# Kernel tuning notes

Hardware: AMD Instinct MI355X
Metric: run time of the kernel (lower is better)

Reference implementation:

```python
import jax, jax.numpy as jnp
import numpy as np

B, T, V, E, H, DE = 64, 52, 10000, 512, 512, 2048


def _lstm_cell(x, h, c, w_ih, w_hh, b_ih, b_hh):
    # torch.nn.LSTMCell gate order: i, f, g, o
    gates = x @ w_ih.T + h @ w_hh.T + b_ih + b_hh
    i, f, g, o = jnp.split(gates, 4, axis=-1)
    c2 = jax.nn.sigmoid(f) * c + jax.nn.sigmoid(i) * jnp.tanh(g)
    h2 = jax.nn.sigmoid(o) * jnp.tanh(c2)
    return h2, c2


def _run_dir(emb_seq, img, lens, p1, p2, fc_w, fc_b):
    # emb_seq: [B, Td, E]; img: [B, H]; lens: [B] sorted descending.
    # The torch loop slices h[:batch_size_t]; since lens is sorted descending,
    # that is equivalent to masking updates where t >= (len-1). Rows that fall
    # out of the active prefix are never read again, and their predictions stay 0.
    Bd, Td = emb_seq.shape[0], emb_seq.shape[1]
    Hd = img.shape[1]
    mask = jnp.arange(Td)[None, :] < (lens - 1)[:, None]  # [B, Td]
    z = jnp.zeros((Bd, Hd), emb_seq.dtype)

    def step(carry, xs):
        h, c, h1, c1 = carry
        x, m = xs
        m2 = m[:, None]
        hn, cn = _lstm_cell(x, h, c, *p1)
        h1n, c1n = _lstm_cell(jnp.concatenate([hn, img], axis=1), h1, c1, *p2)
        carry = (jnp.where(m2, hn, h), jnp.where(m2, cn, c),
                 jnp.where(m2, h1n, h1), jnp.where(m2, c1n, c1))
        preds = jnp.where(m2, h1n @ fc_w.T + fc_b, 0.0)  # [B, V]
        return carry, preds

    _, preds = jax.lax.scan(step, (z, z, z, z), (emb_seq.transpose(1, 0, 2), mask.T))
    return preds.transpose(1, 0, 2)  # [B, Td, V]


def setup_inputs():
    key = jax.random.key(0)
    ks = iter(jax.random.split(key, 48))

    def u(shape, a=-0.1, b=0.1):
        return jax.random.uniform(next(ks), shape, minval=a, maxval=b, dtype=jnp.float32)

    inp = {}
    inp['encoder_out'] = jax.random.normal(next(ks), (B, DE), dtype=jnp.float32)
    inp['encoded_captions'] = jax.random.randint(next(ks), (B, T), 0, V)
    cl = jax.random.randint(next(ks), (B, 1), 2, T + 1)
    inp['caption_lengths'] = cl.at[0, 0].set(T)  # ensure max decode length = T-1
    # embeddings (uniform -0.1..0.1 per init_weights)
    inp['emb_w'] = u((V, E))
    inp['emb_r_w'] = u((V, E))
    # LSTM cells: torch default init uniform(-1/sqrt(H), 1/sqrt(H))
    kH = 1.0 / np.sqrt(H)
    for name, din in [('1', E), ('2', 2 * H), ('r1', E), ('r2', 2 * H)]:
        inp['w_ih' + name] = u((4 * H, din), -kH, kH)
        inp['w_hh' + name] = u((4 * H, H), -kH, kH)
        inp['b_ih' + name] = u((4 * H,), -kH, kH)
        inp['b_hh' + name] = u((4 * H,), -kH, kH)
    kD = 1.0 / np.sqrt(DE)
    inp['img_f_w'] = u((H, DE), -kD, kD)
    inp['img_f_b'] = u((H,), -kD, kD)
    inp['img_b_w'] = u((H, DE), -kD, kD)
    inp['img_b_b'] = u((H,), -kD, kD)
    inp['fc_w'] = u((V, H))
    inp['fc_b'] = jnp.zeros((V,), jnp.float32)
    inp['fcr_w'] = u((V, H))
    inp['fcr_b'] = jnp.zeros((V,), jnp.float32)
    return inp


def reference(encoder_out, encoded_captions, caption_lengths, emb_w, emb_r_w,
              w_ih1, w_hh1, b_ih1, b_hh1, w_ih2, w_hh2, b_ih2, b_hh2,
              w_ihr1, w_hhr1, b_ihr1, b_hhr1, w_ihr2, w_hhr2, b_ihr2, b_hhr2,
              img_f_w, img_f_b, img_b_w, img_b_b, fc_w, fc_b, fcr_w, fcr_b):
    lens = caption_lengths[:, 0]
    order = jnp.argsort(-lens)  # descending, stable (jax argsort is stable)
    lens = lens[order]
    enc = encoder_out[order]
    caps = encoded_captions[order]
    Tc = caps.shape[1]
    # per-row reversal of the first len tokens; rest zero (matches torch loop)
    j = jnp.arange(Tc)[None, :]
    valid = j < lens[:, None]
    rev_idx = jnp.where(valid, lens[:, None] - 1 - j, 0)
    caps_rev = jnp.where(valid, jnp.take_along_axis(caps, rev_idx, axis=1), 0)
    emb = emb_w[caps]          # [B, T, E]
    emb_r = emb_r_w[caps_rev]  # [B, T, E]
    img_f = enc @ img_f_w.T + img_f_b
    img_r = enc @ img_b_w.T + img_b_b
    Td = Tc - 1  # max(decode_lengths); setup guarantees max(lens) == T
    preds = _run_dir(emb[:, :Td], img_f, lens,
                     (w_ih1, w_hh1, b_ih1, b_hh1), (w_ih2, w_hh2, b_ih2, b_hh2), fc_w, fc_b)
    preds_r = _run_dir(emb_r[:, :Td], img_r, lens,
                       (w_ihr1, w_hhr1, b_ihr1, b_hhr1), (w_ihr2, w_hhr2, b_ihr2, b_hhr2), fcr_w, fcr_b)
    return preds, preds_r, caps, caps_rev, lens - 1, order
```

## Files before the change

kernel.cpp:

```cpp
#include <hip/hip_runtime.h>
#include <stdint.h>

#define B64   64
#define T52   52
#define TD    51
#define V10K  10000
#define MP    3328
#define MR    3264
#define NPFC  10112

typedef float  f32x4  __attribute__((ext_vector_type(4)));
typedef __bf16 bf16x8 __attribute__((ext_vector_type(8)));
typedef unsigned int u32x4 __attribute__((ext_vector_type(4)));
typedef unsigned short ushort_t;

__device__ inline unsigned short f2bf(float f) {
  unsigned u = __builtin_bit_cast(unsigned, f);
  u += 0x7fffu + ((u >> 16) & 1u);
  return (unsigned short)(u >> 16);
}
__device__ inline unsigned pack2(float a, float b) {
  return (unsigned)f2bf(a) | ((unsigned)f2bf(b) << 16);
}
__device__ inline float sigm(float x) { return 1.f / (1.f + expf(-x)); }

__device__ inline void store2_sc(ushort_t* p, unsigned v) {
  asm volatile("global_store_short %0, %1, off sc1" :: "v"(p), "v"(v) : "memory");
}
__device__ inline void loadA16(const ushort_t* a, u32x4 (&h)[16]) {
  asm volatile(
    "global_load_dwordx4 %0,  %16, off sc1\n\t"
    "global_load_dwordx4 %1,  %16, off offset:64 sc1\n\t"
    "global_load_dwordx4 %2,  %16, off offset:128 sc1\n\t"
    "global_load_dwordx4 %3,  %16, off offset:192 sc1\n\t"
    "global_load_dwordx4 %4,  %16, off offset:256 sc1\n\t"
    "global_load_dwordx4 %5,  %16, off offset:320 sc1\n\t"
    "global_load_dwordx4 %6,  %16, off offset:384 sc1\n\t"
    "global_load_dwordx4 %7,  %16, off offset:448 sc1\n\t"
    "global_load_dwordx4 %8,  %16, off offset:512 sc1\n\t"
    "global_load_dwordx4 %9,  %16, off offset:576 sc1\n\t"
    "global_load_dwordx4 %10, %16, off offset:640 sc1\n\t"
    "global_load_dwordx4 %11, %16, off offset:704 sc1\n\t"
    "global_load_dwordx4 %12, %16, off offset:768 sc1\n\t"
    "global_load_dwordx4 %13, %16, off offset:832 sc1\n\t"
    "global_load_dwordx4 %14, %16, off offset:896 sc1\n\t"
    "global_load_dwordx4 %15, %16, off offset:960 sc1\n\t"
    "s_waitcnt vmcnt(0)"
    : "=&v"(h[0]),"=&v"(h[1]),"=&v"(h[2]),"=&v"(h[3]),
      "=&v"(h[4]),"=&v"(h[5]),"=&v"(h[6]),"=&v"(h[7]),
      "=&v"(h[8]),"=&v"(h[9]),"=&v"(h[10]),"=&v"(h[11]),
      "=&v"(h[12]),"=&v"(h[13]),"=&v"(h[14]),"=&v"(h[15])
    : "v"(a) : "memory");
}
__device__ inline void loadA32(const ushort_t* a, const ushort_t* b,
                               u32x4 (&ha)[16], u32x4 (&hb)[16]) {
  asm volatile(
    "global_load_dwordx4 %0,  %32, off sc1\n\t"
    "global_load_dwordx4 %1,  %32, off offset:64 sc1\n\t"
    "global_load_dwordx4 %2,  %32, off offset:128 sc1\n\t"
    "global_load_dwordx4 %3,  %32, off offset:192 sc1\n\t"
    "global_load_dwordx4 %4,  %32, off offset:256 sc1\n\t"
    "global_load_dwordx4 %5,  %32, off offset:320 sc1\n\t"
    "global_load_dwordx4 %6,  %32, off offset:384 sc1\n\t"
    "global_load_dwordx4 %7,  %32, off offset:448 sc1\n\t"
    "global_load_dwordx4 %8,  %32, off offset:512 sc1\n\t"
    "global_load_dwordx4 %9,  %32, off offset:576 sc1\n\t"
    "global_load_dwordx4 %10, %32, off offset:640 sc1\n\t"
    "global_load_dwordx4 %11, %32, off offset:704 sc1\n\t"
    "global_load_dwordx4 %12, %32, off offset:768 sc1\n\t"
    "global_load_dwordx4 %13, %32, off offset:832 sc1\n\t"
    "global_load_dwordx4 %14, %32, off offset:896 sc1\n\t"
    "global_load_dwordx4 %15, %32, off offset:960 sc1\n\t"
    "global_load_dwordx4 %16, %33, off sc1\n\t"
    "global_load_dwordx4 %17, %33, off offset:64 sc1\n\t"
    "global_load_dwordx4 %18, %33, off offset:128 sc1\n\t"
    "global_load_dwordx4 %19, %33, off offset:192 sc1\n\t"
    "global_load_dwordx4 %20, %33, off offset:256 sc1\n\t"
    "global_load_dwordx4 %21, %33, off offset:320 sc1\n\t"
    "global_load_dwordx4 %22, %33, off offset:384 sc1\n\t"
    "global_load_dwordx4 %23, %33, off offset:448 sc1\n\t"
    "global_load_dwordx4 %24, %33, off offset:512 sc1\n\t"
    "global_load_dwordx4 %25, %33, off offset:576 sc1\n\t"
    "global_load_dwordx4 %26, %33, off offset:640 sc1\n\t"
    "global_load_dwordx4 %27, %33, off offset:704 sc1\n\t"
    "global_load_dwordx4 %28, %33, off offset:768 sc1\n\t"
    "global_load_dwordx4 %29, %33, off offset:832 sc1\n\t"
    "global_load_dwordx4 %30, %33, off offset:896 sc1\n\t"
    "global_load_dwordx4 %31, %33, off offset:960 sc1\n\t"
    "s_waitcnt vmcnt(0)"
    : "=&v"(ha[0]),"=&v"(ha[1]),"=&v"(ha[2]),"=&v"(ha[3]),
      "=&v"(ha[4]),"=&v"(ha[5]),"=&v"(ha[6]),"=&v"(ha[7]),
      "=&v"(ha[8]),"=&v"(ha[9]),"=&v"(ha[10]),"=&v"(ha[11]),
      "=&v"(ha[12]),"=&v"(ha[13]),"=&v"(ha[14]),"=&v"(ha[15]),
      "=&v"(hb[0]),"=&v"(hb[1]),"=&v"(hb[2]),"=&v"(hb[3]),
      "=&v"(hb[4]),"=&v"(hb[5]),"=&v"(hb[6]),"=&v"(hb[7]),
      "=&v"(hb[8]),"=&v"(hb[9]),"=&v"(hb[10]),"=&v"(hb[11]),
      "=&v"(hb[12]),"=&v"(hb[13]),"=&v"(hb[14]),"=&v"(hb[15])
    : "v"(a), "v"(b) : "memory");
}

__global__ void k_prep(const int* __restrict__ cl, const int* __restrict__ caps,
                       float* __restrict__ out_caps, float* __restrict__ out_capr,
                       float* __restrict__ out_lm1, float* __restrict__ out_ord,
                       int* __restrict__ order_i, int* __restrict__ lensm1_i,
                       int* __restrict__ nvtab, int* __restrict__ capsS,
                       int* __restrict__ capsRev, int* __restrict__ cumtab,
                       int* __restrict__ rowmap)
{
  __shared__ int L[64], O[64], Ls_s[64], Cum[65];
  __shared__ int C_s[64][T52];
  int i = threadIdx.x;
  L[i] = cl[i];
  __syncthreads();
  if (i == 0) {
    for (int a = 0; a < 64; ++a) O[a] = a;
    for (int a = 1; a < 64; ++a) {
      int key = O[a], kl = L[key], b = a - 1;
      while (b >= 0 && L[O[b]] < kl) { O[b + 1] = O[b]; --b; }
      O[b + 1] = key;
    }
  }
  __syncthreads();
  int src = O[i];
  int Ls  = L[src];
  Ls_s[i] = Ls;
  order_i[i]  = src;
  lensm1_i[i] = Ls - 1;
  out_lm1[i]  = (float)(Ls - 1);
  out_ord[i]  = (float)src;
  for (int t = 0; t < T52; ++t) {
    int c = caps[src * T52 + t];
    C_s[i][t] = c;
    capsS[i * T52 + t]    = c;
    out_caps[i * T52 + t] = (float)c;
  }
  __syncthreads();
  for (int j = 0; j < T52; ++j) {
    int rv = (j < Ls) ? C_s[i][Ls - 1 - j] : 0;
    capsRev[i * T52 + j]  = rv;
    out_capr[i * T52 + j] = (float)rv;
  }
  if (i == 0) {
    int s = 0;
    for (int b = 0; b < 64; ++b) { Cum[b] = s; s += Ls_s[b] - 1; }
    Cum[64] = s;
  }
  __syncthreads();
  cumtab[i] = Cum[i];
  if (i == 0) cumtab[64] = Cum[64];
  for (int t = 0; t < Ls - 1; ++t) rowmap[Cum[i] + t] = i * TD + t;
  if (i < TD) {
    int nv = 0;
    for (int r = 0; r < 64; ++r) nv += (Ls_s[r] - 1 > i) ? 1 : 0;
    nvtab[i] = nv;
  }
}

__global__ void k_convert(const float* __restrict__ w_ih1, const float* __restrict__ w_ihr1,
                          const float* __restrict__ fc_w, const float* __restrict__ fcr_w,
                          const float* __restrict__ b_ih1, const float* __restrict__ b_hh1,
                          const float* __restrict__ b_ihr1, const float* __restrict__ b_hhr1,
                          const float* __restrict__ w_hh1, const float* __restrict__ w_hhr1,
                          const float* __restrict__ w_ih2, const float* __restrict__ w_ihr2,
                          const float* __restrict__ w_hh2, const float* __restrict__ w_hhr2,
                          const float* __restrict__ img_f_w, const float* __restrict__ img_b_w,
                          const float* __restrict__ b_ih2, const float* __restrict__ b_hh2,
                          const float* __restrict__ b_ihr2, const float* __restrict__ b_hhr2,
                          const float* __restrict__ enc, const int* __restrict__ order_i,
                          ushort_t* __restrict__ wih1bf, ushort_t* __restrict__ fcwbf,
                          ushort_t* __restrict__ whh1bf, ushort_t* __restrict__ wih2Lbf,
                          ushort_t* __restrict__ whh2bf, ushort_t* __restrict__ wih2Ibf,
                          ushort_t* __restrict__ imgwbf, ushort_t* __restrict__ encbf,
                          float* __restrict__ biasg1, float* __restrict__ biasg2)
{
  long long gid = (long long)blockIdx.x * blockDim.x + threadIdx.x;
  const long long C1 = 2048LL * 512 / 8;
  const long long CF = (long long)NPFC * 512 / 8;
  const long long bs  = 2 * C1 + 2 * CF;
  const long long bs2 = bs + 6 * C1;
  const long long bs3 = bs2 + 2 * C1;
  const long long bs4 = bs3 + 2 * C1;
  const long long bs5 = bs4 + 32768;
  if (gid < 2 * C1) {
    int dir = gid >= C1; long long cid = gid - (long long)dir * C1;
    const float* s = (dir ? w_ihr1 : w_ih1) + cid * 8;
    ushort_t* d = wih1bf + (long long)dir * 2048 * 512 + cid * 8;
    uint4 v;
    v.x = pack2(s[0], s[1]); v.y = pack2(s[2], s[3]);
    v.z = pack2(s[4], s[5]); v.w = pack2(s[6], s[7]);
    *(uint4*)d = v;
  } else if (gid < bs) {
    long long g2 = gid - 2 * C1; int dir = g2 >= CF;
    long long cid = g2 - (long long)dir * CF;
    long long row = cid >> 6; int k8 = (int)(cid & 63) * 8;
    ushort_t* d = fcwbf + (long long)dir * NPFC * 512 + row * 512 + k8;
    uint4 v;
    if (row < V10K) {
      const float* s = (dir ? fcr_w : fc_w) + row * 512 + k8;
      v.x = pack2(s[0], s[1]); v.y = pack2(s[2], s[3]);
      v.z = pack2(s[4], s[5]); v.w = pack2(s[6], s[7]);
    } else { v.x = v.y = v.z = v.w = 0u; }
    *(uint4*)d = v;
  } else if (gid < bs2) {
    long long e = gid - bs;
    int arr = (int)(e / (2 * C1));
    long long d2 = e - (long long)arr * 2 * C1;
    int dir = d2 >= C1;
    long long cid = d2 - (long long)dir * C1;
    long long row = cid >> 6; int k8 = (int)(cid & 63) * 8;
    const float* s;
    ushort_t* d;
    if (arr == 0)      { s = (dir ? w_hhr1 : w_hh1) + row * 512  + k8; d = whh1bf; }
    else if (arr == 1) { s = (dir ? w_ihr2 : w_ih2) + row * 1024 + k8; d = wih2Lbf; }
    else               { s = (dir ? w_hhr2 : w_hh2) + row * 512  + k8; d = whh2bf; }
    d += (long long)dir * 2048 * 512 + cid * 8;
    uint4 v;
    v.x = pack2(s[0], s[1]); v.y = pack2(s[2], s[3]);
    v.z = pack2(s[4], s[5]); v.w = pack2(s[6], s[7]);
    *(uint4*)d = v;
  } else if (gid < bs3) {
    long long e = gid - bs2; int dir = e >= C1;
    long long cid = e - (long long)dir * C1;
    long long row = cid >> 6; int k8 = (int)(cid & 63) * 8;
    const float* s = (dir ? w_ihr2 : w_ih2) + row * 1024 + 512 + k8;
    ushort_t* d = wih2Ibf + (long long)dir * 2048 * 512 + cid * 8;
    uint4 v;
    v.x = pack2(s[0], s[1]); v.y = pack2(s[2], s[3]);
    v.z = pack2(s[4], s[5]); v.w = pack2(s[6], s[7]);
    *(uint4*)d = v;
  } else if (gid < bs4) {
    long long e = gid - bs3; int dir = e >= C1;
    long long cid = e - (long long)dir * C1;
    long long row = cid >> 8; int c8 = (int)(cid & 255) * 8;
    const float* s = (dir ? img_b_w : img_f_w) + row * 2048 + c8;
    ushort_t* d = imgwbf + (long long)dir * 512 * 2048 + cid * 8;
    uint4 v;
    v.x = pack2(s[0], s[1]); v.y = pack2(s[2], s[3]);
    v.z = pack2(s[4], s[5]); v.w = pack2(s[6], s[7]);
    *(uint4*)d = v;
  } else if (gid < bs5) {
    long long cid = gid - bs4;
    int m = (int)(cid >> 8); int c8 = (int)(cid & 255) * 8;
    const float* s = enc + (long long)order_i[m & 63] * 2048 + c8;
    ushort_t* d = encbf + cid * 8;
    uint4 v;
    v.x = pack2(s[0], s[1]); v.y = pack2(s[2], s[3]);
    v.z = pack2(s[4], s[5]); v.w = pack2(s[6], s[7]);
    *(uint4*)d = v;
  } else {
    long long g3 = gid - bs5;
    if (g3 < 4096) {
      int dir = g3 >= 2048; int j = (int)(g3 & 2047);
      biasg1[dir * 2048 + j] = dir ? (b_ihr1[j] + b_hhr1[j]) : (b_ih1[j] + b_hh1[j]);
    } else if (g3 < 8192) {
      long long g4 = g3 - 4096;
      int dir = g4 >= 2048; int j = (int)(g4 & 2047);
      biasg2[dir * 2048 + j] = dir ? (b_ihr2[j] + b_hhr2[j]) : (b_ih2[j] + b_hh2[j]);
    }
  }
}

__global__ void k_gather(const float* __restrict__ emb_w, const float* __restrict__ emb_r_w,
                         const int* __restrict__ capsS, const int* __restrict__ capsRev,
                         ushort_t* __restrict__ embA)
{
  long long gid = (long long)blockIdx.x * 256 + threadIdx.x;
  const long long CPD = (long long)MP * 512 / 8;
  if (gid >= 2 * CPD) return;
  int dir = gid >= CPD; long long cid = gid - (long long)dir * CPD;
  int m = (int)(cid >> 6); int k8 = (int)(cid & 63) * 8;
  ushort_t* d = embA + (long long)dir * MP * 512 + (long long)m * 512 + k8;
  uint4 v;
  if (m < MR) {
    int b = m / TD, t = m - b * TD;
    int row = dir ? capsRev[b * T52 + t] : capsS[b * T52 + t];
    const float* s = (dir ? emb_r_w : emb_w) + (long long)row * 512 + k8;
    v.x = pack2(s[0], s[1]); v.y = pack2(s[2], s[3]);
    v.z = pack2(s[4], s[5]); v.w = pack2(s[6], s[7]);
  } else { v.x = v.y = v.z = v.w = 0u; }
  *(uint4*)d = v;
}

template<int MODE>
__global__ __launch_bounds__(256)
void k_gemm(const ushort_t* __restrict__ A0, long long As,
            const ushort_t* __restrict__ B0, long long Bs,
            const float* __restrict__ bias0, const float* __restrict__ bias1,
            void* __restrict__ out0, long long Os,
            int Nreal, int K)
{
  __shared__ ushort_t Ab[128 * 32];
  __shared__ ushort_t Bb[128 * 32];
  int dirz = blockIdx.z;
  const ushort_t* A = A0 + dirz * As;
  const ushort_t* Bm = B0 + dirz * Bs;
  const float* bias = dirz ? bias1 : bias0;
  int tid = threadIdx.x;
  int lane = tid & 63, wid = tid >> 6;
  int wr = wid >> 1, wc = wid & 1;
  long long tm = (long long)blockIdx.x * 128, tn = (long long)blockIdx.y * 128;
  f32x4 acc[4][4] = {};
  int c0 = tid, c1 = tid + 256;
  const ushort_t* Ag0 = A + (tm + (c0 >> 2)) * K + (c0 & 3) * 8;
  const ushort_t* Ag1 = A + (tm + (c1 >> 2)) * K + (c1 & 3) * 8;
  const ushort_t* Bg0 = Bm + (tn + (c0 >> 2)) * K + (c0 & 3) * 8;
  const ushort_t* Bg1 = Bm + (tn + (c1 >> 2)) * K + (c1 & 3) * 8;
  int KK = K >> 5;
  for (int kk = 0; kk < KK; ++kk) {
    uint4 va0 = *(const uint4*)(Ag0 + kk * 32);
    uint4 va1 = *(const uint4*)(Ag1 + kk * 32);
    uint4 vb0 = *(const uint4*)(Bg0 + kk * 32);
    uint4 vb1 = *(const uint4*)(Bg1 + kk * 32);
    __syncthreads();
    *(uint4*)&Ab[c0 * 8] = va0;
    *(uint4*)&Ab[c1 * 8] = va1;
    *(uint4*)&Bb[c0 * 8] = vb0;
    *(uint4*)&Bb[c1 * 8] = vb1;
    __syncthreads();
    int koff = (lane >> 4) * 8;
    bf16x8 av[4], bv[4];
    #pragma unroll
    for (int mi = 0; mi < 4; ++mi)
      av[mi] = *(const bf16x8*)&Ab[(wr * 64 + mi * 16 + (lane & 15)) * 32 + koff];
    #pragma unroll
    for (int ni = 0; ni < 4; ++ni)
      bv[ni] = *(const bf16x8*)&Bb[(wc * 64 + ni * 16 + (lane & 15)) * 32 + koff];
    #pragma unroll
    for (int mi = 0; mi < 4; ++mi)
      #pragma unroll
      for (int ni = 0; ni < 4; ++ni)
        acc[mi][ni] = __builtin_amdgcn_mfma_f32_16x16x32_bf16(av[mi], bv[ni], acc[mi][ni], 0, 0, 0);
  }
  #pragma unroll
  for (int mi = 0; mi < 4; ++mi) {
    #pragma unroll
    for (int rr = 0; rr < 4; ++rr) {
      long long m = tm + wr * 64 + mi * 16 + ((lane >> 4) * 4) + rr;
      if (MODE == 0) {
        float* orow = (float*)out0 + dirz * Os + m * (long long)Nreal;
        #pragma unroll
        for (int ni = 0; ni < 4; ++ni) {
          int n = (int)tn + wc * 64 + ni * 16 + (lane & 15);
          orow[n] = acc[mi][ni][rr] + bias[n];
        }
      } else if (MODE == 2) {
        float bm = bias[m];
        float* orow = (float*)out0 + dirz * Os + m * (long long)Nreal;
        #pragma unroll
        for (int ni = 0; ni < 4; ++ni) {
          int n = (int)tn + wc * 64 + ni * 16 + (lane & 15);
          if (n < Nreal) orow[n] = acc[mi][ni][rr] + bm;
        }
      } else {
        ushort_t* orow = (ushort_t*)out0 + dirz * Os + m * (long long)Nreal;
        #pragma unroll
        for (int ni = 0; ni < 4; ++ni) {
          int n = (int)tn + wc * 64 + ni * 16 + (lane & 15);
          orow[n] = f2bf(acc[mi][ni][rr] + bias[n]);
        }
      }
    }
  }
}

__global__ __launch_bounds__(256)
void k_fc(const ushort_t* __restrict__ A0, const ushort_t* __restrict__ B0,
          const float* __restrict__ bias0, const float* __restrict__ bias1,
          float* __restrict__ out0, const int* __restrict__ rowmap,
          const int* __restrict__ cumtab)
{
  const long long PRED = (long long)MR * V10K;
  int Mc = cumtab[64];
  long long tm = (long long)blockIdx.x * 128;
  if (tm >= Mc) return;
  __shared__ ushort_t Ab[128 * 32];
  __shared__ ushort_t Bb[128 * 32];
  int dirz = blockIdx.z;
  const ushort_t* A = A0 + (long long)dirz * MP * 512;
  const ushort_t* Bm = B0 + (long long)dirz * NPFC * 512;
  const float* bias = dirz ? bias1 : bias0;
  float* out = out0 + (long long)dirz * PRED;
  int tid = threadIdx.x;
  int lane = tid & 63, wid = tid >> 6;
  int wr = wid >> 1, wc = wid & 1;
  long long tn = (long long)blockIdx.y * 128;
  f32x4 acc[4][4] = {};
  int c0 = tid, c1 = tid + 256;
  const ushort_t* Ag0 = A + (tm + (c0 >> 2)) * 512 + (c0 & 3) * 8;
  const ushort_t* Ag1 = A + (tm + (c1 >> 2)) * 512 + (c1 & 3) * 8;
  const ushort_t* Bg0 = Bm + (tn + (c0 >> 2)) * 512 + (c0 & 3) * 8;
  const ushort_t* Bg1 = Bm + (tn + (c1 >> 2)) * 512 + (c1 & 3) * 8;
  for (int kk = 0; kk < 16; ++kk) {
    uint4 va0 = *(const uint4*)(Ag0 + kk * 32);
    uint4 va1 = *(const uint4*)(Ag1 + kk * 32);
    uint4 vb0 = *(const uint4*)(Bg0 + kk * 32);
    uint4 vb1 = *(const uint4*)(Bg1 + kk * 32);
    __syncthreads();
    *(uint4*)&Ab[c0 * 8] = va0;
    *(uint4*)&Ab[c1 * 8] = va1;
    *(uint4*)&Bb[c0 * 8] = vb0;
    *(uint4*)&Bb[c1 * 8] = vb1;
    __syncthreads();
    int koff = (lane >> 4) * 8;
    bf16x8 av[4], bv[4];
    #pragma unroll
    for (int mi = 0; mi < 4; ++mi)
      av[mi] = *(const bf16x8*)&Ab[(wr * 64 + mi * 16 + (lane & 15)) * 32 + koff];
    #pragma unroll
    for (int ni = 0; ni < 4; ++ni)
      bv[ni] = *(const bf16x8*)&Bb[(wc * 64 + ni * 16 + (lane & 15)) * 32 + koff];
    #pragma unroll
    for (int mi = 0; mi < 4; ++mi)
      #pragma unroll
      for (int ni = 0; ni < 4; ++ni)
        acc[mi][ni] = __builtin_amdgcn_mfma_f32_16x16x32_bf16(av[mi], bv[ni], acc[mi][ni], 0, 0, 0);
  }
  #pragma unroll
  for (int mi = 0; mi < 4; ++mi) {
    #pragma unroll
    for (int rr = 0; rr < 4; ++rr) {
      long long c = tm + wr * 64 + mi * 16 + ((lane >> 4) * 4) + rr;
      if (c < Mc) {
        int m = rowmap[c];
        float* orow = out + (long long)m * V10K;
        #pragma unroll
        for (int ni = 0; ni < 4; ++ni) {
          int n = (int)tn + wc * 64 + ni * 16 + (lane & 15);
          if (n < V10K) orow[n] = acc[mi][ni][rr] + bias[n];
        }
      }
    }
  }
}

__global__ __launch_bounds__(256)
void k_zero(float* __restrict__ outF, const int* __restrict__ lensm1_i)
{
  const long long PRED = (long long)MR * V10K;
  int m = blockIdx.x;
  int b = m / TD, t = m - b * TD;
  if (t < lensm1_i[b]) return;
  float4 z = {0.f, 0.f, 0.f, 0.f};
  float* r0 = outF + (long long)m * V10K;
  float* r1 = outF + PRED + (long long)m * V10K;
  for (int i = threadIdx.x; i < 2500; i += 256) {
    ((float4*)r0)[i] = z;
    ((float4*)r1)[i] = z;
  }
}

__global__ __launch_bounds__(256, 1)
void k_rec(const ushort_t* __restrict__ whh1bf, const ushort_t* __restrict__ wih2Lbf,
           const ushort_t* __restrict__ whh2bf, const float* __restrict__ xg1,
           const float* __restrict__ xg2imgT,
           ushort_t* __restrict__ h1hist,
           ushort_t* __restrict__ h2buf,
           ushort_t* __restrict__ h2allbf,
           const int* __restrict__ nvtab, const int* __restrict__ cumtab,
           int* __restrict__ slots)
{
  const int bid = blockIdx.x;
  const bool isL2 = bid >= 64;
  int dir, ht, half;
  if (!isL2) { dir = bid >> 5; ht = bid & 31; half = 0; }
  else { int idx = bid - 64; dir = idx >> 6; int sub = idx & 63; half = sub >> 5; ht = sub & 31; }
  const int tid = threadIdx.x;
  const int lane = tid & 63, mt = tid >> 6;
  const int l15 = lane & 15, l4 = lane >> 4;
  const int jl = ht * 16 + l15;

  __shared__ ushort_t Wl[32768];
  __shared__ ushort_t Wi[32768];
  __shared__ int nv_s[64];
  __shared__ int cum_s[64];

  {
    const ushort_t* src = (isL2 ? whh2bf : whh1bf) + (long long)dir * 2048 * 512;
    #pragma unroll
    for (int i = 0; i < 16; ++i) {
      int c = tid + i * 256;
      int nl = c >> 6;
      int kb = (c & 63) * 16;
      int row = (nl >> 4) * 512 + ht * 16 + (nl & 15);
      u32x4 v = *(const u32x4*)(src + (long long)row * 512 + (long long)(c & 63) * 8);
      *(u32x4*)((char*)Wl + nl * 1024 + (kb ^ ((nl & 7) << 4))) = v;
    }
    if (isL2) {
      const ushort_t* src2 = wih2Lbf + (long long)dir * 2048 * 512;
      #pragma unroll
      for (int i = 0; i < 16; ++i) {
        int c = tid + i * 256;
        int nl = c >> 6;
        int kb = (c & 63) * 16;
        int row = (nl >> 4) * 512 + ht * 16 + (nl & 15);
        u32x4 v = *(const u32x4*)(src2 + (long long)row * 512 + (long long)(c & 63) * 8);
        *(u32x4*)((char*)Wi + nl * 1024 + (kb ^ ((nl & 7) << 4))) = v;
      }
    }
    if (tid < TD) nv_s[tid] = nvtab[tid];
    if (tid < 64) cum_s[tid] = cumtab[tid];
  }
  __syncthreads();

  int* aS = slots + dir * 32;
  int* bS = slots + 64 + dir * 64;

  if (!isL2) {
    const int r0 = mt * 16 + l4 * 4;
    f32x4 creg = {0.f, 0.f, 0.f, 0.f};
    for (int t = 0; t < TD; ++t) {
      bool act = (mt * 16 < nv_s[t]);
      float xs[4][4];
      if (act) {
        #pragma unroll
        for (int rr = 0; rr < 4; ++rr) {
          const float* xr = xg1 + ((long long)dir * MP + (long long)(r0 + rr) * TD + t) * 2048;
          #pragma unroll
          for (int g = 0; g < 4; ++g)
            xs[g][rr] = xr[g * 512 + jl];
        }
      }
      if (t > 0) {
        if (mt == 0) {
          for (;;) {
            int v = __hip_atomic_load(&aS[lane & 31], __ATOMIC_RELAXED, __HIP_MEMORY_SCOPE_AGENT);
            if (__all(v >= t)) break;
          }
        }
        __syncthreads();
      }
      if (act) {
        const ushort_t* hsrc = h1hist + ((long long)t * 2 + dir) * (64 * 512);
        u32x4 hv[16];
        loadA16(hsrc + (long long)(mt * 16 + l15) * 512 + l4 * 8, hv);
        f32x4 acc[4] = {};
        #pragma unroll
        for (int kk = 0; kk < 16; ++kk) {
          bf16x8 av = __builtin_bit_cast(bf16x8, hv[kk]);
          int kb = kk * 64 + l4 * 16;
          #pragma unroll
          for (int g = 0; g < 4; ++g) {
            bf16x8 bv = *(const bf16x8*)((const char*)Wl + (g * 16 + l15) * 1024 + (kb ^ ((l15 & 7) << 4)));
            acc[g] = __builtin_amdgcn_mfma_f32_16x16x32_bf16(av, bv, acc[g], 0, 0, 0);
          }
        }
        ushort_t* hdst = h1hist + ((long long)(t + 1) * 2 + dir) * (64 * 512);
        f32x4 cn;
        #pragma unroll
        for (int rr = 0; rr < 4; ++rr) {
          float gi = acc[0][rr] + xs[0][rr];
          float gf = acc[1][rr] + xs[1][rr];
          float gg = acc[2][rr] + xs[2][rr];
          float go = acc[3][rr] + xs[3][rr];
          float c = sigm(gf) * creg[rr] + sigm(gi) * tanhf(gg);
          float h = sigm(go) * tanhf(c);
          cn[rr] = c;
          store2_sc(hdst + (long long)(r0 + rr) * 512 + jl, (unsigned)f2bf(h));
        }
        creg = cn;
      }
      __syncthreads();
      if (tid == 0)
        __hip_atomic_store(&aS[ht], t + 1, __ATOMIC_RELAXED, __HIP_MEMORY_SCOPE_AGENT);
    }
  } else {
    const int r0 = half * 32 + mt * 16 + l4 * 4;
    f32x4 xv2[4];
    {
      const float* xg = xg2imgT + (long long)dir * (2048 * 64);
      #pragma unroll
      for (int g = 0; g < 4; ++g)
        xv2[g] = *(const f32x4*)(xg + (long long)(g * 512 + jl) * 64 + (half * 32 + (mt & 1) * 16 + l4 * 4));
    }
    f32x4 creg = {0.f, 0.f, 0.f, 0.f};
    for (int t = 0; t < TD; ++t) {
      if (mt == 0) {
        for (;;) {
          int va = __hip_atomic_load(&aS[lane & 31], __ATOMIC_RELAXED, __HIP_MEMORY_SCOPE_AGENT);
          int vb = __hip_atomic_load(&bS[lane], __ATOMIC_RELAXED, __HIP_MEMORY_SCOPE_AGENT);
          if (__all((va >= t + 1) & (vb >= t))) break;
        }
      }
      __syncthreads();
      int nv = nv_s[t];
      if (mt < 2 && half * 32 + mt * 16 < nv) {
        const ushort_t* h1s = h1hist + ((long long)(t + 1) * 2 + dir) * (64 * 512);
        const ushort_t* h2s = h2buf + ((long long)((t + 1) & 1) * 2 + dir) * (64 * 512);
        u32x4 ha[16], hb[16];
        loadA32(h1s + (long long)(half * 32 + mt * 16 + l15) * 512 + l4 * 8,
                h2s + (long long)(half * 32 + mt * 16 + l15) * 512 + l4 * 8, ha, hb);
        f32x4 acc[4] = {};
        #pragma unroll
        for (int kk = 0; kk < 16; ++kk) {
          bf16x8 av = __builtin_bit_cast(bf16x8, ha[kk]);
          int kb = kk * 64 + l4 * 16;
          #pragma unroll
          for (int g = 0; g < 4; ++g) {
            bf16x8 bv = *(const bf16x8*)((const char*)Wi + (g * 16 + l15) * 1024 + (kb ^ ((l15 & 7) << 4)));
            acc[g] = __builtin_amdgcn_mfma_f32_16x16x32_bf16(av, bv, acc[g], 0, 0, 0);
          }
        }
        #pragma unroll
        for (int kk = 0; kk < 16; ++kk) {
          bf16x8 av = __builtin_bit_cast(bf16x8, hb[kk]);
          int kb = kk * 64 + l4 * 16;
          #pragma unroll
          for (int g = 0; g < 4; ++g) {
            bf16x8 bv = *(const bf16x8*)((const char*)Wl + (g * 16 + l15) * 1024 + (kb ^ ((l15 & 7) << 4)));
            acc[g] = __builtin_amdgcn_mfma_f32_16x16x32_bf16(av, bv, acc[g], 0, 0, 0);
          }
        }
        ushort_t* h2n = h2buf + ((long long)(t & 1) * 2 + dir) * (64 * 512);
        ushort_t* h2a = h2allbf + (long long)dir * MP * 512;
        f32x4 cn;
        #pragma unroll
        for (int rr = 0; rr < 4; ++rr) {
          float gi = acc[0][rr] + xv2[0][rr];
          float gf = acc[1][rr] + xv2[1][rr];
          float gg = acc[2][rr] + xv2[2][rr];
          float go = acc[3][rr] + xv2[3][rr];
          float c = sigm(gf) * creg[rr] + sigm(gi) * tanhf(gg);
          float h = sigm(go) * tanhf(c);
          cn[rr] = c;
          ushort_t hbb = f2bf(h);
          store2_sc(h2n + (long long)(r0 + rr) * 512 + jl, (unsigned)hbb);
          if (r0 + rr < nv)
            h2a[((long long)(cum_s[r0 + rr] + t)) * 512 + jl] = hbb;
        }
        creg = cn;
      }
      __syncthreads();
      if (tid == 0)
        __hip_atomic_store(&bS[half * 32 + ht], t + 1, __ATOMIC_RELAXED, __HIP_MEMORY_SCOPE_AGENT);
    }
  }
}

extern "C" void kernel_launch(void* const* d_in, const int* in_sizes, int n_in,
                              void* d_out, int out_size, void* d_ws, size_t ws_size,
                              hipStream_t stream)
{
  const float* enc     = (const float*)d_in[0];
  const int*   caps    = (const int*)d_in[1];
  const int*   cl      = (const int*)d_in[2];
  const float* emb_w   = (const float*)d_in[3];
  const float* emb_r_w = (const float*)d_in[4];
  const float* w_ih1   = (const float*)d_in[5];
  const float* w_hh1   = (const float*)d_in[6];
  const float* b_ih1   = (const float*)d_in[7];
  const float* b_hh1   = (const float*)d_in[8];
  const float* w_ih2   = (const float*)d_in[9];
  const float* w_hh2   = (const float*)d_in[10];
  const float* b_ih2   = (const float*)d_in[11];
  const float* b_hh2   = (const float*)d_in[12];
  const float* w_ihr1  = (const float*)d_in[13];
  const float* w_hhr1  = (const float*)d_in[14];
  const float* b_ihr1  = (const float*)d_in[15];
  const float* b_hhr1  = (const float*)d_in[16];
  const float* w_ihr2  = (const float*)d_in[17];
  const float* w_hhr2  = (const float*)d_in[18];
  const float* b_ihr2  = (const float*)d_in[19];
  const float* b_hhr2  = (const float*)d_in[20];
  const float* img_f_w = (const float*)d_in[21];
  const float* img_f_b = (const float*)d_in[22];
  const float* img_b_w = (const float*)d_in[23];
  const float* img_b_b = (const float*)d_in[24];
  const float* fc_w    = (const float*)d_in[25];
  const float* fc_b    = (const float*)d_in[26];
  const float* fcr_w   = (const float*)d_in[27];
  const float* fcr_b   = (const float*)d_in[28];

  float* outF = (float*)d_out;
  const long long PRED = (long long)MR * V10K;
  float* o_caps = outF + 2 * PRED;
  float* o_capr = o_caps + B64 * T52;
  float* o_lm1  = o_capr + B64 * T52;
  float* o_ord  = o_lm1 + B64;
  float*    xg1       = outF;
  ushort_t* whh1bf    = (ushort_t*)(outF + 27500000);
  ushort_t* wih2Lbf   = (ushort_t*)(outF + 28600000);
  ushort_t* whh2bf    = (ushort_t*)(outF + 29700000);
  ushort_t* h1hist    = (ushort_t*)(outF + 31000000);
  ushort_t* wih2Ibf   = (ushort_t*)(outF + 34600000);
  ushort_t* imgwbf    = (ushort_t*)(outF + 35700000);
  ushort_t* encbf     = (ushort_t*)(outF + 36800000);
  ushort_t* imgbf     = (ushort_t*)(outF + 37000000);

  char* w = (char*)d_ws;
  auto alloc = [&](size_t bytes) -> char* {
    char* p = w; w += (bytes + 255) & ~(size_t)255; return p;
  };
  int*      order_i  = (int*)alloc(64 * 4);
  int*      lensm1_i = (int*)alloc(64 * 4);
  int*      nvtab    = (int*)alloc(64 * 4);
  int*      cumtab   = (int*)alloc(65 * 4);
  int*      rowmap   = (int*)alloc(MR * 4);
  int*      capsS    = (int*)alloc(B64 * T52 * 4);
  int*      capsRev  = (int*)alloc(B64 * T52 * 4);
  float*    biasg1   = (float*)alloc(2 * 2048 * 4);
  float*    biasg2   = (float*)alloc(2 * 2048 * 4);
  float*    xg2imgT  = (float*)alloc((size_t)2 * 2048 * 64 * 4);
  char*     stateBase = alloc(262144 + 1024);
  ushort_t* h2buf = (ushort_t*)stateBase;
  int*      slotp = (int*)(stateBase + 262144);
  ushort_t* embA    = (ushort_t*)alloc((size_t)2 * MP * 512 * 2);
  ushort_t* wih1bf  = (ushort_t*)alloc((size_t)2 * 2048 * 512 * 2);
  ushort_t* fcwbf   = (ushort_t*)alloc((size_t)2 * NPFC * 512 * 2);
  ushort_t* h2allbf = (ushort_t*)alloc((size_t)2 * MP * 512 * 2);

  hipMemsetAsync(stateBase, 0, 262144 + 1024, stream);
  hipMemsetAsync(h1hist, 0, 131072, stream);

  k_prep<<<1, 64, 0, stream>>>(cl, caps, o_caps, o_capr, o_lm1, o_ord,
                               order_i, lensm1_i, nvtab, capsS, capsRev,
                               cumtab, rowmap);
  k_convert<<<11360, 256, 0, stream>>>(w_ih1, w_ihr1, fc_w, fcr_w,
                                       b_ih1, b_hh1, b_ihr1, b_hhr1,
                                       w_hh1, w_hhr1, w_ih2, w_ihr2, w_hh2, w_hhr2,
                                       img_f_w, img_b_w, b_ih2, b_hh2, b_ihr2, b_hhr2,
                                       enc, order_i,
                                       wih1bf, fcwbf, whh1bf, wih2Lbf, whh2bf,
                                       wih2Ibf, imgwbf, encbf, biasg1, biasg2);
  k_gather<<<1664, 256, 0, stream>>>(emb_w, emb_r_w, capsS, capsRev, embA);
  k_gemm<3><<<dim3(1, 4, 2), 256, 0, stream>>>(encbf, 0LL,
                                               imgwbf, 512LL * 2048,
                                               img_f_b, img_b_b,
                                               imgbf, 128LL * 512,
                                               512, 2048);
  k_gemm<2><<<dim3(16, 1, 2), 256, 0, stream>>>(wih2Ibf, 2048LL * 512,
                                                imgbf, 128LL * 512,
                                                biasg2, biasg2 + 2048,
                                                xg2imgT, 2048LL * 64,
                                                64, 512);
  k_gemm<0><<<dim3(26, 16, 2), 256, 0, stream>>>(embA, (long long)MP * 512,
                                                 wih1bf, 2048LL * 512,
                                                 biasg1, biasg1 + 2048,
                                                 xg1, (long long)MP * 2048,
                                                 2048, 512);
  k_rec<<<192, 256, 0, stream>>>(whh1bf, wih2Lbf, whh2bf, xg1, xg2imgT,
                                 h1hist, h2buf, h2allbf, nvtab, cumtab, slotp);
  k_zero<<<MR, 256, 0, stream>>>(outF, lensm1_i);
  k_fc<<<dim3(26, 79, 2), 256, 0, stream>>>(h2allbf, fcwbf, fc_b, fcr_b,
                                            outF, rowmap, cumtab);
}
```

Baseline: 752.0 us.

## Compact embedding rows, skip empty GEMM tiles, split recurrent blocks by batch half

The embedding gather now writes only active (batch, time) rows in compacted order via rowmap/cumtab. The input-projection GEMM exits early for tiles beyond the active row count. The recurrent kernel moves from 192 blocks of 256 threads to 256 blocks of 128 threads. Layer-1 is now split by batch half as well, with per-half sync slots, so each block does less work per step and waits on fewer peers. This removes wasted GEMM work on padded rows and shortens per-step critical work in the recurrence, but adds more blocks that must be co-resident, each holding its own weight tile in LDS.

```diff
diff --git a/kernel.cpp b/kernel.cpp
--- a/kernel.cpp
+++ b/kernel.cpp
@@ -262,16 +262,18 @@
 
 __global__ void k_gather(const float* __restrict__ emb_w, const float* __restrict__ emb_r_w,
                          const int* __restrict__ capsS, const int* __restrict__ capsRev,
+                         const int* __restrict__ rowmap, const int* __restrict__ cumtab,
                          ushort_t* __restrict__ embA)
 {
   long long gid = (long long)blockIdx.x * 256 + threadIdx.x;
   const long long CPD = (long long)MP * 512 / 8;
   if (gid >= 2 * CPD) return;
   int dir = gid >= CPD; long long cid = gid - (long long)dir * CPD;
-  int m = (int)(cid >> 6); int k8 = (int)(cid & 63) * 8;
-  ushort_t* d = embA + (long long)dir * MP * 512 + (long long)m * 512 + k8;
+  int c = (int)(cid >> 6); int k8 = (int)(cid & 63) * 8;
+  ushort_t* d = embA + (long long)dir * MP * 512 + (long long)c * 512 + k8;
   uint4 v;
-  if (m < MR) {
+  if (c < cumtab[64]) {
+    int m = rowmap[c];
     int b = m / TD, t = m - b * TD;
     int row = dir ? capsRev[b * T52 + t] : capsS[b * T52 + t];
     const float* s = (dir ? emb_r_w : emb_w) + (long long)row * 512 + k8;
@@ -287,8 +289,10 @@
             const ushort_t* __restrict__ B0, long long Bs,
             const float* __restrict__ bias0, const float* __restrict__ bias1,
             void* __restrict__ out0, long long Os,
-            int Nreal, int K)
+            int Nreal, int K, const int* __restrict__ mlim)
 {
+  long long tm = (long long)blockIdx.x * 128;
+  if (mlim && tm >= mlim[64]) return;
   __shared__ ushort_t Ab[128 * 32];
   __shared__ ushort_t Bb[128 * 32];
   int dirz = blockIdx.z;
@@ -298,7 +302,7 @@
   int tid = threadIdx.x;
   int lane = tid & 63, wid = tid >> 6;
   int wr = wid >> 1, wc = wid & 1;
-  long long tm = (long long)blockIdx.x * 128, tn = (long long)blockIdx.y * 128;
+  long long tn = (long long)blockIdx.y * 128;
   f32x4 acc[4][4] = {};
   int c0 = tid, c1 = tid + 256;
   const ushort_t* Ag0 = A + (tm + (c0 >> 2)) * K + (c0 & 3) * 8;
@@ -449,7 +453,7 @@
   }
 }
 
-__global__ __launch_bounds__(256, 1)
+__global__ __launch_bounds__(128, 1)
 void k_rec(const ushort_t* __restrict__ whh1bf, const ushort_t* __restrict__ wih2Lbf,
            const ushort_t* __restrict__ whh2bf, const float* __restrict__ xg1,
            const float* __restrict__ xg2imgT,
@@ -460,14 +464,15 @@
            int* __restrict__ slots)
 {
   const int bid = blockIdx.x;
-  const bool isL2 = bid >= 64;
-  int dir, ht, half;
-  if (!isL2) { dir = bid >> 5; ht = bid & 31; half = 0; }
-  else { int idx = bid - 64; dir = idx >> 6; int sub = idx & 63; half = sub >> 5; ht = sub & 31; }
+  const bool isL2 = bid >= 128;
+  const int idx = isL2 ? bid - 128 : bid;
+  const int dir = idx >> 6, sub = idx & 63, half = sub >> 5, ht = sub & 31;
   const int tid = threadIdx.x;
   const int lane = tid & 63, mt = tid >> 6;
   const int l15 = lane & 15, l4 = lane >> 4;
   const int jl = ht * 16 + l15;
+  const int rbase = half * 32 + mt * 16;
+  const int r0 = rbase + l4 * 4;
 
   __shared__ ushort_t Wl[32768];
   __shared__ ushort_t Wi[32768];
@@ -477,8 +482,8 @@
   {
     const ushort_t* src = (isL2 ? whh2bf : whh1bf) + (long long)dir * 2048 * 512;
     #pragma unroll
-    for (int i = 0; i < 16; ++i) {
-      int c = tid + i * 256;
+    for (int i = 0; i < 32; ++i) {
+      int c = tid + i * 128;
       int nl = c >> 6;
       int kb = (c & 63) * 16;
       int row = (nl >> 4) * 512 + ht * 16 + (nl & 15);
@@ -488,8 +493,8 @@
     if (isL2) {
       const ushort_t* src2 = wih2Lbf + (long long)dir * 2048 * 512;
       #pragma unroll
-      for (int i = 0; i < 16; ++i) {
-        int c = tid + i * 256;
+      for (int i = 0; i < 32; ++i) {
+        int c = tid + i * 128;
         int nl = c >> 6;
         int kb = (c & 63) * 16;
         int row = (nl >> 4) * 512 + ht * 16 + (nl & 15);
@@ -502,19 +507,19 @@
   }
   __syncthreads();
 
-  int* aS = slots + dir * 32;
-  int* bS = slots + 64 + dir * 64;
+  int* aS = slots + (dir * 2 + half) * 32;
+  int* bS = slots + 128 + (dir * 2 + half) * 32;
 
   if (!isL2) {
-    const int r0 = mt * 16 + l4 * 4;
     f32x4 creg = {0.f, 0.f, 0.f, 0.f};
     for (int t = 0; t < TD; ++t) {
-      bool act = (mt * 16 < nv_s[t]);
+      bool act = (rbase < nv_s[t]);
       float xs[4][4];
       if (act) {
+        const float* xb = xg1 + (long long)dir * MP * 2048;
         #pragma unroll
         for (int rr = 0; rr < 4; ++rr) {
-          const float* xr = xg1 + ((long long)dir * MP + (long long)(r0 + rr) * TD + t) * 2048;
+          const float* xr = xb + (long long)(cum_s[r0 + rr] + t) * 2048;
           #pragma unroll
           for (int g = 0; g < 4; ++g)
             xs[g][rr] = xr[g * 512 + jl];
@@ -532,7 +537,7 @@
       if (act) {
         const ushort_t* hsrc = h1hist + ((long long)t * 2 + dir) * (64 * 512);
         u32x4 hv[16];
-        loadA16(hsrc + (long long)(mt * 16 + l15) * 512 + l4 * 8, hv);
+        loadA16(hsrc + (long long)(rbase + l15) * 512 + l4 * 8, hv);
         f32x4 acc[4] = {};
         #pragma unroll
         for (int kk = 0; kk < 16; ++kk) {
@@ -564,31 +569,30 @@
         __hip_atomic_store(&aS[ht], t + 1, __ATOMIC_RELAXED, __HIP_MEMORY_SCOPE_AGENT);
     }
   } else {
-    const int r0 = half * 32 + mt * 16 + l4 * 4;
     f32x4 xv2[4];
     {
       const float* xg = xg2imgT + (long long)dir * (2048 * 64);
       #pragma unroll
       for (int g = 0; g < 4; ++g)
-        xv2[g] = *(const f32x4*)(xg + (long long)(g * 512 + jl) * 64 + (half * 32 + (mt & 1) * 16 + l4 * 4));
+        xv2[g] = *(const f32x4*)(xg + (long long)(g * 512 + jl) * 64 + r0);
     }
     f32x4 creg = {0.f, 0.f, 0.f, 0.f};
     for (int t = 0; t < TD; ++t) {
       if (mt == 0) {
         for (;;) {
           int va = __hip_atomic_load(&aS[lane & 31], __ATOMIC_RELAXED, __HIP_MEMORY_SCOPE_AGENT);
-          int vb = __hip_atomic_load(&bS[lane], __ATOMIC_RELAXED, __HIP_MEMORY_SCOPE_AGENT);
+          int vb = __hip_atomic_load(&bS[lane & 31], __ATOMIC_RELAXED, __HIP_MEMORY_SCOPE_AGENT);
           if (__all((va >= t + 1) & (vb >= t))) break;
         }
       }
       __syncthreads();
       int nv = nv_s[t];
-      if (mt < 2 && half * 32 + mt * 16 < nv) {
+      if (rbase < nv) {
         const ushort_t* h1s = h1hist + ((long long)(t + 1) * 2 + dir) * (64 * 512);
         const ushort_t* h2s = h2buf + ((long long)((t + 1) & 1) * 2 + dir) * (64 * 512);
         u32x4 ha[16], hb[16];
-        loadA32(h1s + (long long)(half * 32 + mt * 16 + l15) * 512 + l4 * 8,
-                h2s + (long long)(half * 32 + mt * 16 + l15) * 512 + l4 * 8, ha, hb);
+        loadA32(h1s + (long long)(rbase + l15) * 512 + l4 * 8,
+                h2s + (long long)(rbase + l15) * 512 + l4 * 8, ha, hb);
         f32x4 acc[4] = {};
         #pragma unroll
         for (int kk = 0; kk < 16; ++kk) {
@@ -631,7 +635,7 @@
       }
       __syncthreads();
       if (tid == 0)
-        __hip_atomic_store(&bS[half * 32 + ht], t + 1, __ATOMIC_RELAXED, __HIP_MEMORY_SCOPE_AGENT);
+        __hip_atomic_store(&bS[ht], t + 1, __ATOMIC_RELAXED, __HIP_MEMORY_SCOPE_AGENT);
     }
   }
 }
@@ -721,23 +725,24 @@
                                        enc, order_i,
                                        wih1bf, fcwbf, whh1bf, wih2Lbf, whh2bf,
                                        wih2Ibf, imgwbf, encbf, biasg1, biasg2);
-  k_gather<<<1664, 256, 0, stream>>>(emb_w, emb_r_w, capsS, capsRev, embA);
+  k_gather<<<1664, 256, 0, stream>>>(emb_w, emb_r_w, capsS, capsRev,
+                                     rowmap, cumtab, embA);
   k_gemm<3><<<dim3(1, 4, 2), 256, 0, stream>>>(encbf, 0LL,
                                                imgwbf, 512LL * 2048,
                                                img_f_b, img_b_b,
                                                imgbf, 128LL * 512,
-                                               512, 2048);
+                                               512, 2048, nullptr);
   k_gemm<2><<<dim3(16, 1, 2), 256, 0, stream>>>(wih2Ibf, 2048LL * 512,
                                                 imgbf, 128LL * 512,
                                                 biasg2, biasg2 + 2048,
                                                 xg2imgT, 2048LL * 64,
-                                                64, 512);
+                                                64, 512, nullptr);
   k_gemm<0><<<dim3(26, 16, 2), 256, 0, stream>>>(embA, (long long)MP * 512,
                                                  wih1bf, 2048LL * 512,
                                                  biasg1, biasg1 + 2048,
                                                  xg1, (long long)MP * 2048,
-                                                 2048, 512);
-  k_rec<<<192, 256, 0, stream>>>(whh1bf, wih2Lbf, whh2bf, xg1, xg2imgT,
+                                                 2048, 512, cumtab);
+  k_rec<<<256, 128, 0, stream>>>(whh1bf, wih2Lbf, whh2bf, xg1, xg2imgT,
                                  h1hist, h2buf, h2allbf, nvtab, cumtab, slotp);
   k_zero<<<MR, 256, 0, stream>>>(outF, lensm1_i);
   k_fc<<<dim3(26, 79, 2), 256, 0, stream>>>(h2allbf, fcwbf, fc_b, fcr_b,
```

After: 694.0 us. -7.7%, faster.
